# Kernel optimization log

Measured on AMD Instinct MI355X. Metric: run time of the kernel, lower is better.

Reference implementation:

```python
import jax, jax.numpy as jnp
import numpy as np


def _grid_sample_3d(vol, grid):
    """Trilinear grid_sample, align_corners=True, zeros padding.
    vol: (b, c, D, H, W); grid: (b, D, H, W, 3) with last dim = (x, y, z)
    where x indexes W, y indexes H, z indexes D (torch convention)."""
    b, c, D, H, W = vol.shape
    dt = vol.dtype
    ix = (grid[..., 0] + 1.0) * 0.5 * (W - 1)
    iy = (grid[..., 1] + 1.0) * 0.5 * (H - 1)
    iz = (grid[..., 2] + 1.0) * 0.5 * (D - 1)
    ix0 = jnp.floor(ix); iy0 = jnp.floor(iy); iz0 = jnp.floor(iz)
    fx = ix - ix0; fy = iy - iy0; fz = iz - iz0

    def gather(v, zi, yi, xi):  # v: (c,D,H,W); indices: (D,H,W)
        return v[:, zi, yi, xi]  # -> (c,D,H,W)

    out = jnp.zeros((b, c, D, H, W), dt)
    for dz in (0, 1):
        z = iz0 + dz
        wz = fz if dz else (1.0 - fz)
        vz = (z >= 0) & (z <= D - 1)
        zi = jnp.clip(z, 0, D - 1).astype(jnp.int32)
        for dy in (0, 1):
            yc = iy0 + dy
            wy = fy if dy else (1.0 - fy)
            vy = (yc >= 0) & (yc <= H - 1)
            yi = jnp.clip(yc, 0, H - 1).astype(jnp.int32)
            for dx in (0, 1):
                xc = ix0 + dx
                wx = fx if dx else (1.0 - fx)
                vx = (xc >= 0) & (xc <= W - 1)
                xi = jnp.clip(xc, 0, W - 1).astype(jnp.int32)
                wgt = (wz * wy * wx) * (vz & vy & vx).astype(dt)  # (b,D,H,W)
                vals = jax.vmap(gather)(vol, zi, yi, xi)          # (b,c,D,H,W)
                out = out + vals * wgt[:, None]
    return out


def _forward(x, y):
    b, c, h, w, d = x.shape
    dt = x.dtype
    # identity affine_grid coordinates (align_corners=True):
    # grid[...,0] varies along innermost axis d, [...,1] along w, [...,2] along h
    gx = jnp.linspace(-1.0, 1.0, d, dtype=dt)[None, None, None, :]
    gy = jnp.linspace(-1.0, 1.0, w, dtype=dt)[None, None, :, None]
    gz = jnp.linspace(-1.0, 1.0, h, dtype=dt)[None, :, None, None]

    x0 = x[:, 0]  # (b,h,w,d), channel 0 as in the torch code
    y0 = y[:, 0]
    x_sum = jnp.sum(x)  # global sums, matching torch.sum over all elements
    y_sum = jnp.sum(y)

    tx = jnp.sum(x0 * gx) / x_sum - jnp.sum(y0 * gx) / y_sum
    ty = jnp.sum(x0 * gy) / x_sum - jnp.sum(y0 * gy) / y_sum
    tz = jnp.sum(x0 * gz) / x_sum - jnp.sum(y0 * gz) / y_sum

    shp = (b, h, w, d)
    grid = jnp.stack([
        jnp.broadcast_to(gx + tx, shp),
        jnp.broadcast_to(gy + ty, shp),
        jnp.broadcast_to(gz + tz, shp),
    ], axis=-1)  # (b,h,w,d,3)

    transformed = _grid_sample_3d(x, grid)
    return transformed, grid


def setup_inputs() -> dict:
    key = jax.random.key(0)
    k1, k2 = jax.random.split(key)
    shape = (2, 1, 192, 192, 192)
    x = jax.random.uniform(k1, shape, dtype=jnp.float32)
    y = jax.random.uniform(k2, shape, dtype=jnp.float32)
    return {"x": x, "y": y}


def reference(x, y):
    return _forward(x, y)
```

## Files before the change

kernel.cpp:

```cpp
#include <hip/hip_runtime.h>

typedef float f4 __attribute__((ext_vector_type(4)));

static constexpr int DIM     = 192;
static constexpr int NVOX    = 2 * DIM * DIM * DIM;
static constexpr int N8      = NVOX / 8;
static constexpr int TSIZE   = NVOX;
static constexpr int RBLOCKS = 256;
static constexpr int RTHREADS = 1024;

__global__ __launch_bounds__(1024) void com_reduce(const float* __restrict__ x,
                                                   const float* __restrict__ y,
                                                   float* __restrict__ ws) {
    const float step = 2.0f / 191.0f;
    float a0 = 0, a1 = 0, a2 = 0, a3 = 0;
    float b0 = 0, b1 = 0, b2 = 0, b3 = 0;

    for (int t8 = blockIdx.x * RTHREADS + threadIdx.x; t8 < N8;
         t8 += RBLOCKS * RTHREADS) {
        int idx = t8 * 8;
        int k = idx % DIM;
        int r = idx / DIM;
        int j = r % DIM;
        int i = (r / DIM) % DIM;

        const f4* xp = reinterpret_cast<const f4*>(x) + t8 * 2;
        const f4* yp = reinterpret_cast<const f4*>(y) + t8 * 2;
        f4 x0 = __builtin_nontemporal_load(xp);
        f4 x1 = __builtin_nontemporal_load(xp + 1);
        f4 y0 = __builtin_nontemporal_load(yp);
        f4 y1 = __builtin_nontemporal_load(yp + 1);

        float g[8];
#pragma unroll
        for (int u = 0; u < 8; ++u) g[u] = fmaf((float)(k + u), step, -1.0f);
        float gj = fmaf((float)j, step, -1.0f);
        float gi = fmaf((float)i, step, -1.0f);

        float xs = ((x0.x + x0.y) + (x0.z + x0.w)) + ((x1.x + x1.y) + (x1.z + x1.w));
        float ys = ((y0.x + y0.y) + (y0.z + y0.w)) + ((y1.x + y1.y) + (y1.z + y1.w));
        float xg = ((x0.x * g[0] + x0.y * g[1]) + (x0.z * g[2] + x0.w * g[3]))
                 + ((x1.x * g[4] + x1.y * g[5]) + (x1.z * g[6] + x1.w * g[7]));
        float yg = ((y0.x * g[0] + y0.y * g[1]) + (y0.z * g[2] + y0.w * g[3]))
                 + ((y1.x * g[4] + y1.y * g[5]) + (y1.z * g[6] + y1.w * g[7]));

        a0 += xs;  a1 += xg;  a2 += xs * gj;  a3 += xs * gi;
        b0 += ys;  b1 += yg;  b2 += ys * gj;  b3 += ys * gi;
    }

    float v[8] = {a0, a1, a2, a3, b0, b1, b2, b3};
#pragma unroll
    for (int q = 0; q < 8; ++q) {
#pragma unroll
        for (int off = 32; off > 0; off >>= 1)
            v[q] += __shfl_down(v[q], off, 64);
    }

    __shared__ float sm[16][8];
    int lane = threadIdx.x & 63;
    int wave = threadIdx.x >> 6;
    if (lane == 0) {
#pragma unroll
        for (int q = 0; q < 8; ++q) sm[wave][q] = v[q];
    }
    __syncthreads();
    if (threadIdx.x < 8) {
        float s = 0;
#pragma unroll
        for (int w = 0; w < 16; ++w) s += sm[w][threadIdx.x];
        ws[blockIdx.x * 8 + threadIdx.x] = s;
    }
}

__global__ __launch_bounds__(384) void com_apply(const float* __restrict__ x,
                                                 float* __restrict__ out,
                                                 const float* __restrict__ wsp) {
    __shared__ double sd[6][8];
    __shared__ float  sp[16];
    __shared__ float  srow[9][240];

    int tid = threadIdx.x;

    for (int p = tid; p < 432; p += 384) {
        int m = p / 48, cc = p % 48;
        int col = (cc < 16) ? cc : (cc - 16 + 208);
        srow[m][col] = 0.0f;
    }

    {
        double s = 0;
        for (int idx = tid; idx < RBLOCKS * 8; idx += 384)
            s += (double)wsp[idx];
        s += __shfl_xor(s, 8, 64);
        s += __shfl_xor(s, 16, 64);
        s += __shfl_xor(s, 32, 64);
        int lane = tid & 63, wave = tid >> 6;
        if (lane < 8) sd[wave][lane] = s;
    }
    __syncthreads();
    if (tid == 0) {
        double t[8];
#pragma unroll
        for (int q = 0; q < 8; ++q) {
            double s = 0;
#pragma unroll
            for (int w = 0; w < 6; ++w) s += sd[w][q];
            t[q] = s;
        }
        double tx = t[1] / t[0] - t[5] / t[4];
        double ty = t[2] / t[0] - t[6] / t[4];
        double tz = t[3] / t[0] - t[7] / t[4];
        double sx = tx * 95.5, sy = ty * 95.5, sz = tz * 95.5;
        double fsx = floor(sx), fsy = floor(sy), fsz = floor(sz);
        sp[0] = (float)(sx - fsx);
        sp[1] = (float)(sy - fsy);
        sp[2] = (float)(sz - fsz);
        sp[3] = (float)tx;
        sp[4] = (float)ty;
        sp[5] = (float)tz;
        int* ip = reinterpret_cast<int*>(sp + 6);
        ip[0] = (int)fsx; ip[1] = (int)fsy; ip[2] = (int)fsz;
    }
    __syncthreads();

    float fx = sp[0], fy = sp[1], fz = sp[2];
    float txf = sp[3], tyf = sp[4], tzf = sp[5];
    const int* ip = reinterpret_cast<const int*>(sp + 6);
    int iox = ip[0], ioy = ip[1], ioz = ip[2];

    int bid = blockIdx.x;
    int jg = bid % 24;
    int i  = (bid / 24) % DIM;
    int b  = bid / (24 * DIM);
    int j0 = jg * 8;

    int z0 = i + ioz, z1 = z0 + 1;
    float wz0 = (z0 >= 0 && z0 < DIM) ? 1.0f - fz : 0.0f;
    float wz1 = (z1 >= 0 && z1 < DIM) ? fz : 0.0f;
    int zc0 = min(max(z0, 0), DIM - 1), zc1 = min(max(z1, 0), DIM - 1);

    const float* xb = x + (size_t)b * (DIM * DIM * DIM);
    for (int task = tid; task < 432; task += 384) {
        int m = task / 48;
        int c = (task % 48) * 4;
        int yv = j0 + ioy + m;
        int yc = min(max(yv, 0), DIM - 1);
        const f4* p0 = reinterpret_cast<const f4*>(xb + (zc0 * DIM + yc) * DIM + c);
        const f4* p1 = reinterpret_cast<const f4*>(xb + (zc1 * DIM + yc) * DIM + c);
        f4 va = *p0;
        f4 vb = *p1;
        f4 s = wz0 * va + wz1 * vb;
        *reinterpret_cast<f4*>(&srow[m][16 + c]) = s;
    }
    __syncthreads();

    int rr = tid / 48;
    int k4 = tid % 48;
    int k  = k4 * 4;
    int j  = j0 + rr;
    int yv0 = j + ioy, yv1 = yv0 + 1;
    float wy0 = (yv0 >= 0 && yv0 < DIM) ? 1.0f - fy : 0.0f;
    float wy1 = (yv1 >= 0 && yv1 < DIM) ? fy : 0.0f;

    float wx0[4], wx1[4];
#pragma unroll
    for (int m = 0; m < 4; ++m) {
        int c0 = k + m + iox, c1 = c0 + 1;
        wx0[m] = (c0 >= 0 && c0 < DIM) ? 1.0f - fx : 0.0f;
        wx1[m] = (c1 >= 0 && c1 < DIM) ? fx : 0.0f;
    }

    int a  = iox & 3;
    int cb = 16 + k + (iox - a);
    float f0[8], f1[8];
    *reinterpret_cast<f4*>(&f0[0]) = *reinterpret_cast<const f4*>(&srow[rr][cb]);
    *reinterpret_cast<f4*>(&f0[4]) = *reinterpret_cast<const f4*>(&srow[rr][cb + 4]);
    *reinterpret_cast<f4*>(&f1[0]) = *reinterpret_cast<const f4*>(&srow[rr + 1][cb]);
    *reinterpret_cast<f4*>(&f1[4]) = *reinterpret_cast<const f4*>(&srow[rr + 1][cb + 4]);

    float res[4];
#define DOCASE(A)                                                           \
    _Pragma("unroll")                                                       \
    for (int m = 0; m < 4; ++m) {                                           \
        float u0 = wy0 * f0[A + m]     + wy1 * f1[A + m];                   \
        float u1 = wy0 * f0[A + m + 1] + wy1 * f1[A + m + 1];               \
        res[m] = wx0[m] * u0 + wx1[m] * u1;                                 \
    }
    switch (a) {
        case 0: DOCASE(0); break;
        case 1: DOCASE(1); break;
        case 2: DOCASE(2); break;
        default: DOCASE(3); break;
    }
#undef DOCASE

    f4 tr = {res[0], res[1], res[2], res[3]};
    __builtin_nontemporal_store(tr, reinterpret_cast<f4*>(out) + bid * 384 + tid);

    const float step = 2.0f / 191.0f;
    float gzv = fmaf((float)i, step, -1.0f) + tzf;
    int g4base = TSIZE / 4 + bid * 1152;
#pragma unroll
    for (int s = 0; s < 3; ++s) {
        f4 gv;
#pragma unroll
        for (int u = 0; u < 4; ++u) {
            int L = (tid + s * 384) * 4 + u;
            int lv = L / 3;
            int comp = L - lv * 3;
            int kk = lv % DIM;
            int rj = lv / DIM;
            float val;
            if (comp == 0)      val = fmaf((float)kk, step, -1.0f) + txf;
            else if (comp == 1) val = fmaf((float)(j0 + rj), step, -1.0f) + tyf;
            else                val = gzv;
            gv[u] = val;
        }
        __builtin_nontemporal_store(gv, reinterpret_cast<f4*>(out) + g4base + tid + s * 384);
    }
}

extern "C" void kernel_launch(void* const* d_in, const int* in_sizes, int n_in,
                              void* d_out, int out_size, void* d_ws, size_t ws_size,
                              hipStream_t stream) {
    const float* x = (const float*)d_in[0];
    const float* y = (const float*)d_in[1];
    float* out = (float*)d_out;
    float* ws = (float*)d_ws;

    com_reduce<<<RBLOCKS, RTHREADS, 0, stream>>>(x, y, ws);
    com_apply<<<NVOX / 1536, 384, 0, stream>>>(x, out, ws);
}
```

Measured before the change: 93.65 us.

## Split apply kernel into finalize, sample, and grid-write kernels

The per-block redundant final reduction of partial sums moves into a single-block finalize kernel that writes the translation parameters to workspace. Sampling and grid output become separate kernels, so the sample kernel is lighter and the grid writer runs with its own launch shape. The x loads in the reduction drop the nontemporal hint so x may stay in cache for the sampling pass. The cost is two extra kernel launches and a serial single-block step between them.

```diff
diff --git a/kernel.cpp b/kernel.cpp
--- a/kernel.cpp
+++ b/kernel.cpp
@@ -2,11 +2,11 @@
 
 typedef float f4 __attribute__((ext_vector_type(4)));
 
-static constexpr int DIM     = 192;
-static constexpr int NVOX    = 2 * DIM * DIM * DIM;
-static constexpr int N8      = NVOX / 8;
-static constexpr int TSIZE   = NVOX;
-static constexpr int RBLOCKS = 256;
+static constexpr int DIM      = 192;
+static constexpr int NVOX     = 2 * DIM * DIM * DIM;
+static constexpr int N8       = NVOX / 8;
+static constexpr int TSIZE    = NVOX;
+static constexpr int RBLOCKS  = 256;
 static constexpr int RTHREADS = 1024;
 
 __global__ __launch_bounds__(1024) void com_reduce(const float* __restrict__ x,
@@ -26,8 +26,8 @@
 
         const f4* xp = reinterpret_cast<const f4*>(x) + t8 * 2;
         const f4* yp = reinterpret_cast<const f4*>(y) + t8 * 2;
-        f4 x0 = __builtin_nontemporal_load(xp);
-        f4 x1 = __builtin_nontemporal_load(xp + 1);
+        f4 x0 = xp[0];
+        f4 x1 = xp[1];
         f4 y0 = __builtin_nontemporal_load(yp);
         f4 y1 = __builtin_nontemporal_load(yp + 1);
 
@@ -68,17 +68,50 @@
         float s = 0;
 #pragma unroll
         for (int w = 0; w < 16; ++w) s += sm[w][threadIdx.x];
-        ws[blockIdx.x * 8 + threadIdx.x] = s;
-    }
-}
-
-__global__ __launch_bounds__(384) void com_apply(const float* __restrict__ x,
-                                                 float* __restrict__ out,
-                                                 const float* __restrict__ wsp) {
-    __shared__ double sd[6][8];
-    __shared__ float  sp[16];
-    __shared__ float  srow[9][240];
-
+        ws[16 + blockIdx.x * 8 + threadIdx.x] = s;
+    }
+}
+
+__global__ __launch_bounds__(256) void com_finalize(float* __restrict__ ws) {
+    __shared__ double sd[256];
+    int t = threadIdx.x;
+    int q = t & 7;
+    double s = 0;
+    for (int p = t >> 3; p < RBLOCKS; p += 32)
+        s += (double)ws[16 + p * 8 + q];
+    sd[t] = s;
+    __syncthreads();
+    for (int off = 128; off >= 8; off >>= 1) {
+        if (t < off) sd[t] += sd[t + off];
+        __syncthreads();
+    }
+    if (t == 0) {
+        double xs = sd[0], xgx = sd[1], xgy = sd[2], xgz = sd[3];
+        double ys = sd[4], ygx = sd[5], ygy = sd[6], ygz = sd[7];
+        double tx = xgx / xs - ygx / ys;
+        double ty = xgy / xs - ygy / ys;
+        double tz = xgz / xs - ygz / ys;
+        double sx = tx * 95.5, sy = ty * 95.5, sz = tz * 95.5;
+        double fsx = floor(sx), fsy = floor(sy), fsz = floor(sz);
+        ws[0] = (float)(sx - fsx);
+        ws[1] = (float)(sy - fsy);
+        ws[2] = (float)(sz - fsz);
+        ws[3] = (float)tx;
+        ws[4] = (float)ty;
+        ws[5] = (float)tz;
+        int* ip = reinterpret_cast<int*>(ws + 6);
+        ip[0] = (int)fsx; ip[1] = (int)fsy; ip[2] = (int)fsz;
+    }
+}
+
+__global__ __launch_bounds__(384) void com_sample(const float* __restrict__ x,
+                                                  float* __restrict__ out,
+                                                  const float* __restrict__ ws) {
+    float fx = ws[0], fy = ws[1], fz = ws[2];
+    const int* ip = reinterpret_cast<const int*>(ws + 6);
+    int iox = ip[0], ioy = ip[1], ioz = ip[2];
+
+    __shared__ float srow[9][240];
     int tid = threadIdx.x;
 
     for (int p = tid; p < 432; p += 384) {
@@ -86,47 +119,6 @@
         int col = (cc < 16) ? cc : (cc - 16 + 208);
         srow[m][col] = 0.0f;
     }
-
-    {
-        double s = 0;
-        for (int idx = tid; idx < RBLOCKS * 8; idx += 384)
-            s += (double)wsp[idx];
-        s += __shfl_xor(s, 8, 64);
-        s += __shfl_xor(s, 16, 64);
-        s += __shfl_xor(s, 32, 64);
-        int lane = tid & 63, wave = tid >> 6;
-        if (lane < 8) sd[wave][lane] = s;
-    }
-    __syncthreads();
-    if (tid == 0) {
-        double t[8];
-#pragma unroll
-        for (int q = 0; q < 8; ++q) {
-            double s = 0;
-#pragma unroll
-            for (int w = 0; w < 6; ++w) s += sd[w][q];
-            t[q] = s;
-        }
-        double tx = t[1] / t[0] - t[5] / t[4];
-        double ty = t[2] / t[0] - t[6] / t[4];
-        double tz = t[3] / t[0] - t[7] / t[4];
-        double sx = tx * 95.5, sy = ty * 95.5, sz = tz * 95.5;
-        double fsx = floor(sx), fsy = floor(sy), fsz = floor(sz);
-        sp[0] = (float)(sx - fsx);
-        sp[1] = (float)(sy - fsy);
-        sp[2] = (float)(sz - fsz);
-        sp[3] = (float)tx;
-        sp[4] = (float)ty;
-        sp[5] = (float)tz;
-        int* ip = reinterpret_cast<int*>(sp + 6);
-        ip[0] = (int)fsx; ip[1] = (int)fsy; ip[2] = (int)fsz;
-    }
-    __syncthreads();
-
-    float fx = sp[0], fy = sp[1], fz = sp[2];
-    float txf = sp[3], tyf = sp[4], tzf = sp[5];
-    const int* ip = reinterpret_cast<const int*>(sp + 6);
-    int iox = ip[0], ioy = ip[1], ioz = ip[2];
 
     int bid = blockIdx.x;
     int jg = bid % 24;
@@ -145,12 +137,9 @@
         int c = (task % 48) * 4;
         int yv = j0 + ioy + m;
         int yc = min(max(yv, 0), DIM - 1);
-        const f4* p0 = reinterpret_cast<const f4*>(xb + (zc0 * DIM + yc) * DIM + c);
-        const f4* p1 = reinterpret_cast<const f4*>(xb + (zc1 * DIM + yc) * DIM + c);
-        f4 va = *p0;
-        f4 vb = *p1;
-        f4 s = wz0 * va + wz1 * vb;
-        *reinterpret_cast<f4*>(&srow[m][16 + c]) = s;
+        f4 va = *reinterpret_cast<const f4*>(xb + (zc0 * DIM + yc) * DIM + c);
+        f4 vb = *reinterpret_cast<const f4*>(xb + (zc1 * DIM + yc) * DIM + c);
+        *reinterpret_cast<f4*>(&srow[m][16 + c]) = wz0 * va + wz1 * vb;
     }
     __syncthreads();
 
@@ -196,27 +185,36 @@
 
     f4 tr = {res[0], res[1], res[2], res[3]};
     __builtin_nontemporal_store(tr, reinterpret_cast<f4*>(out) + bid * 384 + tid);
-
+}
+
+__global__ __launch_bounds__(256) void com_grid(float* __restrict__ out,
+                                                const float* __restrict__ ws) {
+    float txf = ws[3], tyf = ws[4], tzf = ws[5];
     const float step = 2.0f / 191.0f;
-    float gzv = fmaf((float)i, step, -1.0f) + tzf;
-    int g4base = TSIZE / 4 + bid * 1152;
+    int tid = threadIdx.x;
+    int bid = blockIdx.x;
+    int g4base = TSIZE / 4 + bid * 768;
+
 #pragma unroll
     for (int s = 0; s < 3; ++s) {
+        int f4idx = bid * 768 + s * 256 + tid;
         f4 gv;
 #pragma unroll
         for (int u = 0; u < 4; ++u) {
-            int L = (tid + s * 384) * 4 + u;
+            int L = f4idx * 4 + u;
             int lv = L / 3;
             int comp = L - lv * 3;
             int kk = lv % DIM;
-            int rj = lv / DIM;
+            int r  = lv / DIM;
+            int jj = r % DIM;
+            int ii = (r / DIM) % DIM;
             float val;
             if (comp == 0)      val = fmaf((float)kk, step, -1.0f) + txf;
-            else if (comp == 1) val = fmaf((float)(j0 + rj), step, -1.0f) + tyf;
-            else                val = gzv;
+            else if (comp == 1) val = fmaf((float)jj, step, -1.0f) + tyf;
+            else                val = fmaf((float)ii, step, -1.0f) + tzf;
             gv[u] = val;
         }
-        __builtin_nontemporal_store(gv, reinterpret_cast<f4*>(out) + g4base + tid + s * 384);
+        __builtin_nontemporal_store(gv, reinterpret_cast<f4*>(out) + g4base + s * 256 + tid);
     }
 }
 
@@ -229,5 +227,7 @@
     float* ws = (float*)d_ws;
 
     com_reduce<<<RBLOCKS, RTHREADS, 0, stream>>>(x, y, ws);
-    com_apply<<<NVOX / 1536, 384, 0, stream>>>(x, out, ws);
-}
+    com_finalize<<<1, 256, 0, stream>>>(ws);
+    com_sample<<<NVOX / 1536, 384, 0, stream>>>(x, out, ws);
+    com_grid<<<(3 * NVOX / 4) / 768, 256, 0, stream>>>(out, ws);
+}
```

Result: faster. 90.27 us (median of 2 runs) (-3.6%).

## Fuse reduction and resampling into one cooperative kernel with grid sync

Applied to the files above, without the earlier changes.

Merges the centre-of-mass reduction and the trilinear apply into a single cooperative launch of 256 blocks of 1024 threads, separated by a grid-wide sync. Each block then handles 12 tiles of 24 rows, staging z-interpolated rows in a larger shared buffer. The reduction now reads float4 instead of float8 per thread, x is read with normal cached loads (possibly so it stays in cache for the apply phase), and output stores are no longer nontemporal. The aim is to remove the second launch and the gap between kernels, and to gain reuse from larger tiles. The cost is that the apply phase is limited to one 1024-thread block per CU, with serial load, sync and compute steps inside each tile.

```diff
diff --git a/kernel.cpp b/kernel.cpp
--- a/kernel.cpp
+++ b/kernel.cpp
@@ -1,115 +1,100 @@
 #include <hip/hip_runtime.h>
+#include <hip/hip_cooperative_groups.h>
+
+namespace cg = cooperative_groups;
 
 typedef float f4 __attribute__((ext_vector_type(4)));
 
 static constexpr int DIM     = 192;
 static constexpr int NVOX    = 2 * DIM * DIM * DIM;
-static constexpr int N8      = NVOX / 8;
+static constexpr int N4      = NVOX / 4;
 static constexpr int TSIZE   = NVOX;
-static constexpr int RBLOCKS = 256;
-static constexpr int RTHREADS = 1024;
-
-__global__ __launch_bounds__(1024) void com_reduce(const float* __restrict__ x,
-                                                   const float* __restrict__ y,
-                                                   float* __restrict__ ws) {
+static constexpr int GRID    = 256;
+static constexpr int THREADS = 1024;
+static constexpr int TOT     = GRID * THREADS;
+
+__global__ __launch_bounds__(1024, 1) void com_fused(const float* __restrict__ x,
+                                                     const float* __restrict__ y,
+                                                     float* __restrict__ out,
+                                                     float* __restrict__ ws) {
+    __shared__ float  sm[16][8];
+    __shared__ double sd[256];
+    __shared__ float  sp[16];
+    __shared__ float  srow[25][240];
+
+    const int tid = threadIdx.x;
+    const int bid = blockIdx.x;
     const float step = 2.0f / 191.0f;
-    float a0 = 0, a1 = 0, a2 = 0, a3 = 0;
-    float b0 = 0, b1 = 0, b2 = 0, b3 = 0;
-
-    for (int t8 = blockIdx.x * RTHREADS + threadIdx.x; t8 < N8;
-         t8 += RBLOCKS * RTHREADS) {
-        int idx = t8 * 8;
-        int k = idx % DIM;
-        int r = idx / DIM;
-        int j = r % DIM;
-        int i = (r / DIM) % DIM;
-
-        const f4* xp = reinterpret_cast<const f4*>(x) + t8 * 2;
-        const f4* yp = reinterpret_cast<const f4*>(y) + t8 * 2;
-        f4 x0 = __builtin_nontemporal_load(xp);
-        f4 x1 = __builtin_nontemporal_load(xp + 1);
-        f4 y0 = __builtin_nontemporal_load(yp);
-        f4 y1 = __builtin_nontemporal_load(yp + 1);
-
-        float g[8];
-#pragma unroll
-        for (int u = 0; u < 8; ++u) g[u] = fmaf((float)(k + u), step, -1.0f);
-        float gj = fmaf((float)j, step, -1.0f);
-        float gi = fmaf((float)i, step, -1.0f);
-
-        float xs = ((x0.x + x0.y) + (x0.z + x0.w)) + ((x1.x + x1.y) + (x1.z + x1.w));
-        float ys = ((y0.x + y0.y) + (y0.z + y0.w)) + ((y1.x + y1.y) + (y1.z + y1.w));
-        float xg = ((x0.x * g[0] + x0.y * g[1]) + (x0.z * g[2] + x0.w * g[3]))
-                 + ((x1.x * g[4] + x1.y * g[5]) + (x1.z * g[6] + x1.w * g[7]));
-        float yg = ((y0.x * g[0] + y0.y * g[1]) + (y0.z * g[2] + y0.w * g[3]))
-                 + ((y1.x * g[4] + y1.y * g[5]) + (y1.z * g[6] + y1.w * g[7]));
-
-        a0 += xs;  a1 += xg;  a2 += xs * gj;  a3 += xs * gi;
-        b0 += ys;  b1 += yg;  b2 += ys * gj;  b3 += ys * gi;
-    }
-
-    float v[8] = {a0, a1, a2, a3, b0, b1, b2, b3};
-#pragma unroll
-    for (int q = 0; q < 8; ++q) {
-#pragma unroll
-        for (int off = 32; off > 0; off >>= 1)
-            v[q] += __shfl_down(v[q], off, 64);
-    }
-
-    __shared__ float sm[16][8];
-    int lane = threadIdx.x & 63;
-    int wave = threadIdx.x >> 6;
-    if (lane == 0) {
-#pragma unroll
-        for (int q = 0; q < 8; ++q) sm[wave][q] = v[q];
+
+    {
+        float a0 = 0, a1 = 0, a2 = 0, a3 = 0;
+        float b0 = 0, b1 = 0, b2 = 0, b3 = 0;
+        for (int t4 = bid * THREADS + tid; t4 < N4; t4 += TOT) {
+            int idx = t4 * 4;
+            int k = idx % DIM;
+            int j = (idx / DIM) % DIM;
+            int i = (idx / (DIM * DIM)) % DIM;
+
+            f4 xv = reinterpret_cast<const f4*>(x)[t4];
+            f4 yv = __builtin_nontemporal_load(reinterpret_cast<const f4*>(y) + t4);
+
+            float g0 = fmaf((float)(k + 0), step, -1.0f);
+            float g1 = fmaf((float)(k + 1), step, -1.0f);
+            float g2 = fmaf((float)(k + 2), step, -1.0f);
+            float g3 = fmaf((float)(k + 3), step, -1.0f);
+            float gj = fmaf((float)j, step, -1.0f);
+            float gi = fmaf((float)i, step, -1.0f);
+
+            float xs = (xv.x + xv.y) + (xv.z + xv.w);
+            float ys = (yv.x + yv.y) + (yv.z + yv.w);
+            float xg = (xv.x * g0 + xv.y * g1) + (xv.z * g2 + xv.w * g3);
+            float yg = (yv.x * g0 + yv.y * g1) + (yv.z * g2 + yv.w * g3);
+
+            a0 += xs;  a1 += xg;  a2 += xs * gj;  a3 += xs * gi;
+            b0 += ys;  b1 += yg;  b2 += ys * gj;  b3 += ys * gi;
+        }
+
+        float v[8] = {a0, a1, a2, a3, b0, b1, b2, b3};
+#pragma unroll
+        for (int q = 0; q < 8; ++q) {
+#pragma unroll
+            for (int off = 32; off > 0; off >>= 1)
+                v[q] += __shfl_down(v[q], off, 64);
+        }
+        int lane = tid & 63, wave = tid >> 6;
+        if (lane == 0) {
+#pragma unroll
+            for (int q = 0; q < 8; ++q) sm[wave][q] = v[q];
+        }
+        __syncthreads();
+        if (tid < 8) {
+            float s = 0;
+#pragma unroll
+            for (int w = 0; w < 16; ++w) s += sm[w][tid];
+            ws[16 + bid * 8 + tid] = s;
+        }
+    }
+
+    cg::this_grid().sync();
+
+    if (tid < 256) {
+        int q = tid & 7;
+        double s = 0;
+        for (int p = tid >> 3; p < GRID; p += 32)
+            s += (double)ws[16 + p * 8 + q];
+        sd[tid] = s;
     }
     __syncthreads();
-    if (threadIdx.x < 8) {
-        float s = 0;
-#pragma unroll
-        for (int w = 0; w < 16; ++w) s += sm[w][threadIdx.x];
-        ws[blockIdx.x * 8 + threadIdx.x] = s;
-    }
-}
-
-__global__ __launch_bounds__(384) void com_apply(const float* __restrict__ x,
-                                                 float* __restrict__ out,
-                                                 const float* __restrict__ wsp) {
-    __shared__ double sd[6][8];
-    __shared__ float  sp[16];
-    __shared__ float  srow[9][240];
-
-    int tid = threadIdx.x;
-
-    for (int p = tid; p < 432; p += 384) {
-        int m = p / 48, cc = p % 48;
-        int col = (cc < 16) ? cc : (cc - 16 + 208);
-        srow[m][col] = 0.0f;
-    }
-
-    {
-        double s = 0;
-        for (int idx = tid; idx < RBLOCKS * 8; idx += 384)
-            s += (double)wsp[idx];
-        s += __shfl_xor(s, 8, 64);
-        s += __shfl_xor(s, 16, 64);
-        s += __shfl_xor(s, 32, 64);
-        int lane = tid & 63, wave = tid >> 6;
-        if (lane < 8) sd[wave][lane] = s;
-    }
-    __syncthreads();
+    for (int off = 128; off >= 8; off >>= 1) {
+        if (tid < off) sd[tid] += sd[tid + off];
+        __syncthreads();
+    }
     if (tid == 0) {
-        double t[8];
-#pragma unroll
-        for (int q = 0; q < 8; ++q) {
-            double s = 0;
-#pragma unroll
-            for (int w = 0; w < 6; ++w) s += sd[w][q];
-            t[q] = s;
-        }
-        double tx = t[1] / t[0] - t[5] / t[4];
-        double ty = t[2] / t[0] - t[6] / t[4];
-        double tz = t[3] / t[0] - t[7] / t[4];
+        double xs = sd[0], xgx = sd[1], xgy = sd[2], xgz = sd[3];
+        double ys = sd[4], ygx = sd[5], ygy = sd[6], ygz = sd[7];
+        double tx = xgx / xs - ygx / ys;
+        double ty = xgy / xs - ygy / ys;
+        double tz = xgz / xs - ygz / ys;
         double sx = tx * 95.5, sy = ty * 95.5, sz = tz * 95.5;
         double fsx = floor(sx), fsy = floor(sy), fsz = floor(sz);
         sp[0] = (float)(sx - fsx);
@@ -121,64 +106,66 @@
         int* ip = reinterpret_cast<int*>(sp + 6);
         ip[0] = (int)fsx; ip[1] = (int)fsy; ip[2] = (int)fsz;
     }
+    for (int p = tid; p < 1200; p += THREADS) {
+        int m = p / 48, cc = p % 48;
+        int col = (cc < 16) ? cc : (cc + 192);
+        srow[m][col] = 0.0f;
+    }
     __syncthreads();
 
-    float fx = sp[0], fy = sp[1], fz = sp[2];
-    float txf = sp[3], tyf = sp[4], tzf = sp[5];
-    const int* ip = reinterpret_cast<const int*>(sp + 6);
-    int iox = ip[0], ioy = ip[1], ioz = ip[2];
-
-    int bid = blockIdx.x;
-    int jg = bid % 24;
-    int i  = (bid / 24) % DIM;
-    int b  = bid / (24 * DIM);
-    int j0 = jg * 8;
-
-    int z0 = i + ioz, z1 = z0 + 1;
-    float wz0 = (z0 >= 0 && z0 < DIM) ? 1.0f - fz : 0.0f;
-    float wz1 = (z1 >= 0 && z1 < DIM) ? fz : 0.0f;
-    int zc0 = min(max(z0, 0), DIM - 1), zc1 = min(max(z1, 0), DIM - 1);
-
-    const float* xb = x + (size_t)b * (DIM * DIM * DIM);
-    for (int task = tid; task < 432; task += 384) {
-        int m = task / 48;
-        int c = (task % 48) * 4;
-        int yv = j0 + ioy + m;
-        int yc = min(max(yv, 0), DIM - 1);
-        const f4* p0 = reinterpret_cast<const f4*>(xb + (zc0 * DIM + yc) * DIM + c);
-        const f4* p1 = reinterpret_cast<const f4*>(xb + (zc1 * DIM + yc) * DIM + c);
-        f4 va = *p0;
-        f4 vb = *p1;
-        f4 s = wz0 * va + wz1 * vb;
-        *reinterpret_cast<f4*>(&srow[m][16 + c]) = s;
-    }
-    __syncthreads();
-
-    int rr = tid / 48;
-    int k4 = tid % 48;
-    int k  = k4 * 4;
-    int j  = j0 + rr;
-    int yv0 = j + ioy, yv1 = yv0 + 1;
-    float wy0 = (yv0 >= 0 && yv0 < DIM) ? 1.0f - fy : 0.0f;
-    float wy1 = (yv1 >= 0 && yv1 < DIM) ? fy : 0.0f;
-
-    float wx0[4], wx1[4];
-#pragma unroll
-    for (int m = 0; m < 4; ++m) {
-        int c0 = k + m + iox, c1 = c0 + 1;
-        wx0[m] = (c0 >= 0 && c0 < DIM) ? 1.0f - fx : 0.0f;
-        wx1[m] = (c1 >= 0 && c1 < DIM) ? fx : 0.0f;
-    }
-
-    int a  = iox & 3;
-    int cb = 16 + k + (iox - a);
-    float f0[8], f1[8];
-    *reinterpret_cast<f4*>(&f0[0]) = *reinterpret_cast<const f4*>(&srow[rr][cb]);
-    *reinterpret_cast<f4*>(&f0[4]) = *reinterpret_cast<const f4*>(&srow[rr][cb + 4]);
-    *reinterpret_cast<f4*>(&f1[0]) = *reinterpret_cast<const f4*>(&srow[rr + 1][cb]);
-    *reinterpret_cast<f4*>(&f1[4]) = *reinterpret_cast<const f4*>(&srow[rr + 1][cb + 4]);
-
-    float res[4];
+    const float fx = sp[0], fy = sp[1], fz = sp[2];
+    const float txf = sp[3], tyf = sp[4], tzf = sp[5];
+    const int* ipp = reinterpret_cast<const int*>(sp + 6);
+    const int iox = ipp[0], ioy = ipp[1], ioz = ipp[2];
+    const int a = iox & 3;
+
+    for (int it = 0; it < 12; ++it) {
+        int tt = bid * 12 + it;
+        int jg = tt % 8;
+        int i  = (tt / 8) % DIM;
+        int b  = tt / (8 * DIM);
+        int j0 = jg * 24;
+
+        int z0 = i + ioz, z1 = z0 + 1;
+        float wz0 = (z0 >= 0 && z0 < DIM) ? 1.0f - fz : 0.0f;
+        float wz1 = (z1 >= 0 && z1 < DIM) ? fz : 0.0f;
+        int zc0 = min(max(z0, 0), DIM - 1), zc1 = min(max(z1, 0), DIM - 1);
+        const float* xb = x + (size_t)b * (DIM * DIM * DIM);
+
+        for (int p = tid; p < 1200; p += THREADS) {
+            int m = p / 48;
+            int c = (p % 48) * 4;
+            int yv = j0 + ioy + m;
+            int yc = min(max(yv, 0), DIM - 1);
+            f4 va = *reinterpret_cast<const f4*>(xb + (zc0 * DIM + yc) * DIM + c);
+            f4 vb = *reinterpret_cast<const f4*>(xb + (zc1 * DIM + yc) * DIM + c);
+            *reinterpret_cast<f4*>(&srow[m][16 + c]) = wz0 * va + wz1 * vb;
+        }
+        __syncthreads();
+
+        for (int q = tid; q < 1152; q += THREADS) {
+            int rr = q / 48, k4 = q % 48, k = k4 * 4;
+            int j = j0 + rr;
+            int yv0 = j + ioy, yv1 = yv0 + 1;
+            float wy0 = (yv0 >= 0 && yv0 < DIM) ? 1.0f - fy : 0.0f;
+            float wy1 = (yv1 >= 0 && yv1 < DIM) ? fy : 0.0f;
+
+            float wx0[4], wx1[4];
+#pragma unroll
+            for (int m = 0; m < 4; ++m) {
+                int c0 = k + m + iox, c1 = c0 + 1;
+                wx0[m] = (c0 >= 0 && c0 < DIM) ? 1.0f - fx : 0.0f;
+                wx1[m] = (c1 >= 0 && c1 < DIM) ? fx : 0.0f;
+            }
+
+            int cb = 16 + k + (iox - a);
+            float f0[8], f1[8];
+            *reinterpret_cast<f4*>(&f0[0]) = *reinterpret_cast<const f4*>(&srow[rr][cb]);
+            *reinterpret_cast<f4*>(&f0[4]) = *reinterpret_cast<const f4*>(&srow[rr][cb + 4]);
+            *reinterpret_cast<f4*>(&f1[0]) = *reinterpret_cast<const f4*>(&srow[rr + 1][cb]);
+            *reinterpret_cast<f4*>(&f1[4]) = *reinterpret_cast<const f4*>(&srow[rr + 1][cb + 4]);
+
+            float res[4];
 #define DOCASE(A)                                                           \
     _Pragma("unroll")                                                       \
     for (int m = 0; m < 4; ++m) {                                           \
@@ -186,37 +173,40 @@
         float u1 = wy0 * f0[A + m + 1] + wy1 * f1[A + m + 1];               \
         res[m] = wx0[m] * u0 + wx1[m] * u1;                                 \
     }
-    switch (a) {
-        case 0: DOCASE(0); break;
-        case 1: DOCASE(1); break;
-        case 2: DOCASE(2); break;
-        default: DOCASE(3); break;
-    }
+            switch (a) {
+                case 0: DOCASE(0); break;
+                case 1: DOCASE(1); break;
+                case 2: DOCASE(2); break;
+                default: DOCASE(3); break;
+            }
 #undef DOCASE
 
-    f4 tr = {res[0], res[1], res[2], res[3]};
-    __builtin_nontemporal_store(tr, reinterpret_cast<f4*>(out) + bid * 384 + tid);
-
-    const float step = 2.0f / 191.0f;
-    float gzv = fmaf((float)i, step, -1.0f) + tzf;
-    int g4base = TSIZE / 4 + bid * 1152;
-#pragma unroll
-    for (int s = 0; s < 3; ++s) {
-        f4 gv;
-#pragma unroll
-        for (int u = 0; u < 4; ++u) {
-            int L = (tid + s * 384) * 4 + u;
-            int lv = L / 3;
-            int comp = L - lv * 3;
-            int kk = lv % DIM;
-            int rj = lv / DIM;
-            float val;
-            if (comp == 0)      val = fmaf((float)kk, step, -1.0f) + txf;
-            else if (comp == 1) val = fmaf((float)(j0 + rj), step, -1.0f) + tyf;
-            else                val = gzv;
-            gv[u] = val;
-        }
-        __builtin_nontemporal_store(gv, reinterpret_cast<f4*>(out) + g4base + tid + s * 384);
+            f4 tr = {res[0], res[1], res[2], res[3]};
+            reinterpret_cast<f4*>(out)[((b * DIM + i) * DIM + j) * 48 + k4] = tr;
+        }
+
+        {
+            float gzv = fmaf((float)i, step, -1.0f) + tzf;
+            int vox0 = ((b * DIM + i) * DIM + j0) * DIM;
+            int base4 = TSIZE / 4 + (vox0 / 4) * 3;
+            for (int g = tid; g < 3456; g += THREADS) {
+                f4 gv;
+#pragma unroll
+                for (int u = 0; u < 4; ++u) {
+                    int L = g * 4 + u;
+                    int lv = L / 3, comp = L - lv * 3;
+                    int kk = lv % DIM;
+                    int jr = lv / DIM;
+                    float val;
+                    if (comp == 0)      val = fmaf((float)kk, step, -1.0f) + txf;
+                    else if (comp == 1) val = fmaf((float)(j0 + jr), step, -1.0f) + tyf;
+                    else                val = gzv;
+                    gv[u] = val;
+                }
+                reinterpret_cast<f4*>(out)[base4 + g] = gv;
+            }
+        }
+        __syncthreads();
     }
 }
 
@@ -228,6 +218,7 @@
     float* out = (float*)d_out;
     float* ws = (float*)d_ws;
 
-    com_reduce<<<RBLOCKS, RTHREADS, 0, stream>>>(x, y, ws);
-    com_apply<<<NVOX / 1536, 384, 0, stream>>>(x, out, ws);
+    void* args[] = {(void*)&x, (void*)&y, (void*)&out, (void*)&ws};
+    hipLaunchCooperativeKernel((void*)com_fused, dim3(GRID), dim3(THREADS),
+                               args, 0, stream);
 }
```

New measurement: 113.7 us. 1.21x slower.
